# Optimization experiments

Hardware: AMD Instinct MI355X
Metric: run time of the kernel (lower is better)

The kernel has to match this reference:

```python
import jax, jax.numpy as jnp
import numpy as np

D_STATE = 16
D_CONV = 4
DT_RANK = 8


def layer_norm(x, g, b, eps=1e-5):
    m = x.mean(-1, keepdims=True)
    v = ((x - m) ** 2).mean(-1, keepdims=True)
    return (x - m) / jnp.sqrt(v + eps) * g + b


def rms_norm(x, w, eps=1e-5):
    return x * jax.lax.rsqrt(jnp.mean(x * x, -1, keepdims=True) + eps) * w


def mamba_layer(feat, in_proj_w, conv_w, conv_b, x_proj_w, dt_proj_w, dt_proj_b,
                A_log, D_param, out_proj_w, rms_w):
    # feat: [N, C] treated as a length-N sequence with batch 1 (residual block)
    x_in = rms_norm(feat, rms_w)
    xz = x_in @ in_proj_w                         # [N, 2*d_inner]
    d_inner = conv_w.shape[0]
    x, z = xz[:, :d_inner], xz[:, d_inner:]
    # causal depthwise conv1d (torch pad=d_conv-1 then truncate to L)
    L = x.shape[0]
    x_pad = jnp.pad(x, ((D_CONV - 1, 0), (0, 0)))
    xc = conv_b + sum(x_pad[k:k + L, :] * conv_w[:, k] for k in range(D_CONV))
    x = jax.nn.silu(xc)
    dbc = x @ x_proj_w                            # [N, dt_rank + 2*d_state]
    delta = jax.nn.softplus(dbc[:, :DT_RANK] @ dt_proj_w + dt_proj_b)  # [N, d_inner]
    Bm = dbc[:, DT_RANK:DT_RANK + D_STATE]        # [N, d_state]
    Cm = dbc[:, DT_RANK + D_STATE:]               # [N, d_state]
    A = -jnp.exp(A_log)                           # [d_inner, d_state]

    def step(h, inp):
        d_t, b_t, c_t, x_t = inp
        dA = jnp.exp(d_t[:, None] * A)            # [d_inner, d_state]
        h = dA * h + d_t[:, None] * b_t[None, :] * x_t[:, None]
        y_t = (h * c_t[None, :]).sum(-1)          # [d_inner]
        return h, y_t

    h0 = jnp.zeros((d_inner, D_STATE), feat.dtype)
    _, y = jax.lax.scan(step, h0, (delta, Bm, Cm, x))
    y = y + D_param * x
    y = y * jax.nn.silu(z)
    return feat + y @ out_proj_w                  # residual


def setup_inputs() -> dict:
    N, K, C = 32768, 16, 128
    d_inner = 2 * C
    key = jax.random.key(0)
    ks = jax.random.split(key, 12)
    s = 0.02
    inp = {
        "feat": jax.random.normal(ks[0], (N, C), jnp.float32),
        "coord": jax.random.normal(ks[1], (N, 3), jnp.float32),
        "reference_index": jax.random.randint(ks[2], (N, K), 0, N, jnp.int32),
        "gauss_dist": jax.random.uniform(ks[3], (N, K), jnp.float32),
        "j": 0,
        # Mamba params
        "in_proj_w": jax.random.normal(ks[4], (C, 2 * d_inner), jnp.float32) * s,
        "conv_w": jax.random.normal(ks[5], (d_inner, D_CONV), jnp.float32) * s,
        "conv_b": jnp.zeros((d_inner,), jnp.float32),
        "x_proj_w": jax.random.normal(ks[6], (d_inner, DT_RANK + 2 * D_STATE), jnp.float32) * s,
        "dt_proj_w": jax.random.normal(ks[7], (DT_RANK, d_inner), jnp.float32) * s,
        "dt_proj_b": jax.random.uniform(ks[8], (d_inner,), jnp.float32) * 0.1,
        "A_log": jnp.log(jnp.tile(jnp.arange(1.0, D_STATE + 1.0, dtype=jnp.float32), (d_inner, 1))),
        "D_param": jnp.ones((d_inner,), jnp.float32),
        "out_proj_w": jax.random.normal(ks[9], (d_inner, C), jnp.float32) * s,
        "rms_w": jnp.ones((C,), jnp.float32),
        # PointBatchNorm (LayerNorm) shared for both norms
        "ln_g": jnp.ones((C,), jnp.float32),
        "ln_b": jnp.zeros((C,), jnp.float32),
        # linear_attention: Linear(2C->C), LayerNorm, ReLU, Linear(C->C)
        "la_w1": jax.random.normal(ks[10], (2 * C, C), jnp.float32) * s,
        "la_b1": jnp.zeros((C,), jnp.float32),
        "la_ln_g": jnp.ones((C,), jnp.float32),
        "la_ln_b": jnp.zeros((C,), jnp.float32),
        "la_w2": jax.random.normal(ks[11], (C, C), jnp.float32) * s,
        "la_b2": jnp.zeros((C,), jnp.float32),
    }
    return inp


def reference(feat, coord, reference_index, gauss_dist, j,
              in_proj_w, conv_w, conv_b, x_proj_w, dt_proj_w, dt_proj_b,
              A_log, D_param, out_proj_w, rms_w, ln_g, ln_b,
              la_w1, la_b1, la_ln_g, la_ln_b, la_w2, la_b2):
    # pointops.grouping(with_xyz=False): gather neighbor features [N, K, C]
    group_feat = feat[reference_index]
    combined = (gauss_dist[..., None] * group_feat).sum(axis=1)     # [N, C]
    combined = layer_norm(combined, ln_g, ln_b)
    feat_mamba = mamba_layer(feat, in_proj_w, conv_w, conv_b, x_proj_w,
                             dt_proj_w, dt_proj_b, A_log, D_param,
                             out_proj_w, rms_w)
    feat_mamba = layer_norm(feat_mamba, ln_g, ln_b)
    cat_feat = jnp.concatenate([feat_mamba, combined], axis=-1)     # [N, 2C]
    h = jax.nn.relu(layer_norm(cat_feat @ la_w1 + la_b1, la_ln_g, la_ln_b))
    return h @ la_w2 + la_b2
```

## Files before the change

kernel.cpp:

```cpp
#include <hip/hip_runtime.h>
#include <hip/hip_bf16.h>
#include <math.h>

#define N_TOK 32768
#define LC 32
#define NCHUNK (N_TOK / LC)
#define NSEG 64
#define SEGLEN (NCHUNK / NSEG)
#define CXT 16
#define NCXB (N_TOK / CXT)
#define XPAD 264

typedef short short8 __attribute__((ext_vector_type(8)));
typedef float f32x4 __attribute__((ext_vector_type(4)));

__device__ __forceinline__ float siluf_(float v){ return v / (1.f + __expf(-v)); }
__device__ __forceinline__ float softplusf_(float v){ return v > 20.f ? v : __logf(1.f + __expf(v)); }

__device__ __forceinline__ unsigned f2bfu(float f){
  __hip_bfloat16 h = __float2bfloat16(f);
  return (unsigned)*(unsigned short*)&h;
}
__device__ __forceinline__ float bfu2f(unsigned short u){
  __hip_bfloat16 h; *(unsigned short*)&h = u; return __bfloat162float(h);
}

__device__ __forceinline__ float waveRed64(float v){
  #pragma unroll
  for (int m = 1; m < 64; m <<= 1) v += __shfl_xor(v, m);
  return v;
}

__device__ __forceinline__ void pow_chain(float w, float pw[16]){
  pw[0]=w; pw[1]=w*w; pw[2]=pw[1]*w; pw[3]=pw[1]*pw[1];
  pw[4]=pw[3]*pw[0]; pw[5]=pw[3]*pw[1]; pw[6]=pw[3]*pw[2]; pw[7]=pw[3]*pw[3];
  pw[8]=pw[7]*pw[0]; pw[9]=pw[7]*pw[1]; pw[10]=pw[7]*pw[2]; pw[11]=pw[7]*pw[3];
  pw[12]=pw[7]*pw[4]; pw[13]=pw[7]*pw[5]; pw[14]=pw[7]*pw[6]; pw[15]=pw[7]*pw[7];
}

__device__ __forceinline__ bool check_intA(const float aS[16]){
  bool ok = true;
  #pragma unroll
  for (int s=0;s<16;s++){
    float tgt = (float)(s+1);
    if (fabsf(-aS[s] - tgt) > 1e-4f*tgt) ok = false;
  }
  return ok;
}

__global__ void __launch_bounds__(256) k_front(const float* __restrict__ feat,
                        const float* __restrict__ rmsw,
                        unsigned* __restrict__ a0u, unsigned* __restrict__ fb16u,
                        const float* __restrict__ ipw, const float* __restrict__ opw,
                        const float* __restrict__ w1, const float* __restrict__ w2,
                        const float* __restrict__ xpw,
                        __hip_bfloat16* __restrict__ ipwt, __hip_bfloat16* __restrict__ opwt,
                        __hip_bfloat16* __restrict__ w1t, __hip_bfloat16* __restrict__ w2t,
                        __hip_bfloat16* __restrict__ xpwt){
  int bid = blockIdx.x;
  if (bid >= 8192){
    int e = (bid-8192)*256 + threadIdx.x;
    if (e < 65536){ int n=e>>7, k=e&127; ipwt[e]=__float2bfloat16(ipw[k*512+n]); }
    else if (e < 98304){ int f=e-65536; int n=f>>8, k=f&255; opwt[f]=__float2bfloat16(opw[k*128+n]); }
    else if (e < 131072){ int f=e-98304; int n=f>>8, k=f&255; w1t[f]=__float2bfloat16(w1[k*128+n]); }
    else if (e < 147456){ int f=e-131072; int n=f>>7, k=f&127; w2t[f]=__float2bfloat16(w2[k*128+n]); }
    else if (e < 159744){ int f=e-147456; int n=f>>8, k=f&255;
                          xpwt[f]=(n<40)?__float2bfloat16(xpw[k*40+n]):__float2bfloat16(0.f); }
    return;
  }
  int row = bid*4 + (threadIdx.x>>6);
  int lane = threadIdx.x & 63;
  float2 f2 = ((const float2*)feat)[row*64 + lane];
  fb16u[row*64 + lane] = f2bfu(f2.x) | (f2bfu(f2.y) << 16);
  float ss = waveRed64(f2.x*f2.x + f2.y*f2.y);
  float is0 = rsqrtf(ss * (1.f/128.f) + 1e-5f);
  float2 w = ((const float2*)rmsw)[lane];
  a0u[row*64 + lane] = f2bfu(f2.x*is0*w.x) | (f2bfu(f2.y*is0*w.y) << 16);
}

template<int WM16, int WN16>
__global__ __launch_bounds__(256) void k_mfma(const __hip_bfloat16* __restrict__ A,
      const __hip_bfloat16* __restrict__ Wt, int K,
      __hip_bfloat16* __restrict__ out0b, __hip_bfloat16* __restrict__ out1){
  int tid = threadIdx.x;
  int wave = tid>>6, lane = tid&63;
  int wm = wave>>1, wn = wave&1;
  int lane16 = lane&15, quad = lane>>4;
  int m_w = blockIdx.x*(2*WM16*16) + wm*(WM16*16);
  int n_w = blockIdx.y*(2*WN16*16) + wn*(WN16*16);
  f32x4 acc[WM16][WN16];
  #pragma unroll
  for (int i=0;i<WM16;i++)
    #pragma unroll
    for (int j=0;j<WN16;j++) acc[i][j] = (f32x4){0.f,0.f,0.f,0.f};
  const __hip_bfloat16* Ab = A  + (size_t)(m_w + lane16)*K + quad*8;
  const __hip_bfloat16* Bb = Wt + (size_t)(n_w + lane16)*K + quad*8;
  #pragma unroll 4
  for (int kk=0; kk<K; kk+=32){
    short8 a[WM16], b[WN16];
    #pragma unroll
    for (int i=0;i<WM16;i++) a[i] = *(const short8*)(Ab + (size_t)i*16*K + kk);
    #pragma unroll
    for (int j=0;j<WN16;j++) b[j] = *(const short8*)(Bb + (size_t)j*16*K + kk);
    #pragma unroll
    for (int i=0;i<WM16;i++)
      #pragma unroll
      for (int j=0;j<WN16;j++)
        acc[i][j] = __builtin_amdgcn_mfma_f32_16x16x32_bf16(b[j], a[i], acc[i][j], 0, 0, 0);
  }
  #pragma unroll
  for (int i=0;i<WM16;i++){
    int m = m_w + i*16 + lane16;
    #pragma unroll
    for (int j=0;j<WN16;j++){
      int n0 = n_w + j*16 + quad*4;
      if (n0 < 256){
        unsigned u0 = f2bfu(acc[i][j][0]) | (f2bfu(acc[i][j][1]) << 16);
        unsigned u1 = f2bfu(acc[i][j][2]) | (f2bfu(acc[i][j][3]) << 16);
        *(uint2*)(out0b + (size_t)m*256 + n0) = make_uint2(u0, u1);
      } else {
        unsigned u0 = f2bfu(siluf_(acc[i][j][0])) | (f2bfu(siluf_(acc[i][j][1])) << 16);
        unsigned u1 = f2bfu(siluf_(acc[i][j][2])) | (f2bfu(siluf_(acc[i][j][3])) << 16);
        *(uint2*)(out1 + (size_t)m*256 + (n0-256)) = make_uint2(u0, u1);
      }
    }
  }
}

__global__ __launch_bounds__(256) void k_cxd(
      const __hip_bfloat16* __restrict__ bxb,
      const __hip_bfloat16* __restrict__ xpwt,
      const float* __restrict__ cw, const float* __restrict__ cb,
      const float* __restrict__ dtw, const float* __restrict__ dtb,
      unsigned* __restrict__ dxb,
      float* __restrict__ Bm, float* __restrict__ Cm,
      const unsigned* __restrict__ fb16u, const int* __restrict__ ridx,
      const float* __restrict__ gd, const float* __restrict__ g,
      const float* __restrict__ b, unsigned* __restrict__ catB){
  int tid = threadIdx.x;
  int bid = blockIdx.x;

  if (bid >= NCXB){
    int row = (bid - NCXB)*4 + (tid>>6);
    int lane = tid & 63;
    float ax=0.f, ay=0.f;
    #pragma unroll 4
    for (int k=0;k<16;k++){
      int idx = ridx[row*16+k];
      float ww = gd[row*16+k];
      unsigned fu = fb16u[(size_t)idx*64 + lane];
      ax += ww*bfu2f((unsigned short)(fu & 0xffff));
      ay += ww*bfu2f((unsigned short)(fu >> 16));
    }
    float m = waveRed64(ax+ay) * (1.f/128.f);
    float dx = ax-m, dy = ay-m;
    float var = waveRed64(dx*dx+dy*dy) * (1.f/128.f);
    float is = rsqrtf(var + 1e-5f);
    float2 gg = ((const float2*)g)[lane];
    float2 bb = ((const float2*)b)[lane];
    float ox = dx*is*gg.x + bb.x, oy = dy*is*gg.y + bb.y;
    catB[row*64 + lane] = f2bfu(ox) | (f2bfu(oy) << 16);
    return;
  }

  __shared__ __align__(16) __hip_bfloat16 Xs[CXT][XPAD];
  __shared__ __align__(16) float DT[CXT][8];
  int wave = tid>>6, lane = tid&63;
  int lane16 = lane&15, quad = lane>>4;
  int r0 = bid*CXT;

  {
    int d = tid;
    float cw0=cw[d*4], cw1=cw[d*4+1], cw2=cw[d*4+2], cw3=cw[d*4+3], cbb=cb[d];
    float a_0 = (r0 >= 3) ? __bfloat162float(bxb[(size_t)(r0-3)*256 + d]) : 0.f;
    float a_1 = (r0 >= 2) ? __bfloat162float(bxb[(size_t)(r0-2)*256 + d]) : 0.f;
    float a_2 = (r0 >= 1) ? __bfloat162float(bxb[(size_t)(r0-1)*256 + d]) : 0.f;
    #pragma unroll 4
    for (int t=0;t<CXT;t++){
      float a_3 = __bfloat162float(bxb[(size_t)(r0+t)*256 + d]);
      float xc = siluf_(cbb + cw0*a_0 + cw1*a_1 + cw2*a_2 + cw3*a_3);
      Xs[t][d] = __float2bfloat16(xc);
      a_0=a_1; a_1=a_2; a_2=a_3;
    }
  }
  __syncthreads();

  if (wave < 3){
    f32x4 acc3 = (f32x4){0.f,0.f,0.f,0.f};
    const __hip_bfloat16* Arow = &Xs[lane16][0] + quad*8;
    const __hip_bfloat16* Bb = xpwt + (size_t)(wave*16 + lane16)*256 + quad*8;
    #pragma unroll
    for (int kk=0; kk<256; kk+=32){
      short8 a  = *(const short8*)(Arow + kk);
      short8 bfr = *(const short8*)(Bb + kk);
      acc3 = __builtin_amdgcn_mfma_f32_16x16x32_bf16(a, bfr, acc3, 0, 0, 0);
    }
    int n = wave*16 + lane16;
    #pragma unroll
    for (int r=0;r<4;r++){
      int m = quad*4 + r;
      float v = acc3[r];
      if (n < 8)       DT[m][n] = v;
      else if (n < 24) Bm[(size_t)(r0+m)*16 + (n-8)] = v;
      else if (n < 40) Cm[(size_t)(r0+m)*16 + (n-24)] = v;
    }
  }
  __syncthreads();

  {
    int d = tid;
    float w8[8];
    #pragma unroll
    for (int j=0;j<8;j++) w8[j] = dtw[j*256+d];
    float dbias = dtb[d];
    #pragma unroll
    for (int t=0;t<CXT;t++){
      const float4* T = (const float4*)&DT[t][0];
      float4 u = T[0], v = T[1];
      float acc = dbias
        + u.x*w8[0] + u.y*w8[1] + u.z*w8[2] + u.w*w8[3]
        + v.x*w8[4] + v.y*w8[5] + v.z*w8[6] + v.w*w8[7];
      float dv = softplusf_(acc);
      unsigned xu = *(const unsigned short*)&Xs[t][d];
      dxb[(size_t)(r0+t)*256 + d] = f2bfu(dv) | (xu << 16);
    }
  }
}

__global__ __launch_bounds__(256) void k_scan1(const unsigned* __restrict__ dxb,
      const float* __restrict__ Bm, const float* __restrict__ A_log,
      float* __restrict__ dsum_o, __hip_bfloat16* __restrict__ Hc){
  __shared__ float Bl[LC][16];
  int g = blockIdx.x;
  int tid = threadIdx.x;
  int d = tid;
  int t0 = g*LC;
  if (tid < LC*4) ((float4*)&Bl[0][0])[tid] = ((const float4*)(Bm + (size_t)t0*16))[tid];
  __syncthreads();
  float aS[16];
  #pragma unroll
  for (int s=0;s<16;s++) aS[s] = -__expf(A_log[d*16+s]);
  bool fastA = check_intA(aS);
  float h[16] = {};
  float dsum = 0.f;
  if (fastA){
    #pragma unroll 4
    for (int t=0;t<LC;t++){
      unsigned u = dxb[(size_t)(t0+t)*256 + d];
      float dv = bfu2f((unsigned short)(u & 0xffff));
      float xv = bfu2f((unsigned short)(u >> 16));
      const float4* Bp = (const float4*)&Bl[t][0];
      float4 b0=Bp[0], b1=Bp[1], b2=Bp[2], b3=Bp[3];
      float bl[16] = {b0.x,b0.y,b0.z,b0.w, b1.x,b1.y,b1.z,b1.w,
                      b2.x,b2.y,b2.z,b2.w, b3.x,b3.y,b3.z,b3.w};
      dsum += dv;
      float dx_ = dv*xv;
      float w[16]; pow_chain(__expf(-dv), w);
      #pragma unroll
      for (int s=0;s<16;s++) h[s] = w[s]*h[s] + dx_*bl[s];
    }
  } else {
    #pragma unroll 4
    for (int t=0;t<LC;t++){
      unsigned u = dxb[(size_t)(t0+t)*256 + d];
      float dv = bfu2f((unsigned short)(u & 0xffff));
      float xv = bfu2f((unsigned short)(u >> 16));
      const float4* Bp = (const float4*)&Bl[t][0];
      float4 b0=Bp[0], b1=Bp[1], b2=Bp[2], b3=Bp[3];
      float bl[16] = {b0.x,b0.y,b0.z,b0.w, b1.x,b1.y,b1.z,b1.w,
                      b2.x,b2.y,b2.z,b2.w, b3.x,b3.y,b3.z,b3.w};
      dsum += dv;
      float dx_ = dv*xv;
      #pragma unroll
      for (int s=0;s<16;s++) h[s] = __expf(dv*aS[s])*h[s] + dx_*bl[s];
    }
  }
  dsum_o[(size_t)g*256 + d] = dsum;
  unsigned u[8];
  #pragma unroll
  for (int q=0;q<8;q++) u[q] = f2bfu(h[2*q]) | (f2bfu(h[2*q+1]) << 16);
  uint4* Hd = (uint4*)(Hc + (size_t)g*4096 + (size_t)d*16);
  Hd[0] = make_uint4(u[0],u[1],u[2],u[3]);
  Hd[1] = make_uint4(u[4],u[5],u[6],u[7]);
}

__global__ __launch_bounds__(256) void k_carry_a(const float* __restrict__ dsum,
      __hip_bfloat16* __restrict__ Hc, const float* __restrict__ A_log,
      float* __restrict__ dsum_pre, float* __restrict__ segsum, float* __restrict__ Hagg){
  int seg = blockIdx.x;
  int ch  = blockIdx.y*256 + threadIdx.x;
  int d = ch>>4, s = ch&15;
  float aSv = -__expf(A_log[ch]);
  float dpre = 0.f, c = 0.f;
  int g0 = seg*SEGLEN;
  #pragma unroll 4
  for (int i=0;i<SEGLEN;i++){
    int g = g0+i;
    float ds = dsum[(size_t)g*256 + d];
    size_t a = (size_t)g*4096 + ch;
    float hh = __bfloat162float(Hc[a]);
    float p = __expf(ds*aSv);
    if (s==0) dsum_pre[(size_t)g*256 + d] = dpre;
    Hc[a] = __float2bfloat16(c);
    dpre += ds;
    c = p*c + hh;
  }
  if (s==0) segsum[seg*256 + d] = dpre;
  Hagg[(size_t)seg*4096 + ch] = c;
}

__global__ __launch_bounds__(256) void k_carry_b(const float* __restrict__ segsum,
      const float* __restrict__ Hagg, const float* __restrict__ A_log,
      float* __restrict__ Cseg){
  int ch = blockIdx.x*256 + threadIdx.x;
  int d = ch>>4;
  float aSv = -__expf(A_log[ch]);
  float c = 0.f;
  #pragma unroll 8
  for (int s=0;s<NSEG;s++){
    Cseg[(size_t)s*4096 + ch] = c;
    c = __expf(segsum[s*256 + d]*aSv)*c + Hagg[(size_t)s*4096 + ch];
  }
}

__global__ __launch_bounds__(256) void k_scan2(const unsigned* __restrict__ dxb,
      const __hip_bfloat16* __restrict__ zb, const float* __restrict__ Bm,
      const float* __restrict__ Cm, const float* __restrict__ A_log,
      const float* __restrict__ Dp, const float* __restrict__ dsum_pre,
      const __hip_bfloat16* __restrict__ Hc, const float* __restrict__ Cseg,
      __hip_bfloat16* __restrict__ yb){
  __shared__ float Bl[LC][16];
  __shared__ float Cl[LC][16];
  int g = blockIdx.x;
  int tid = threadIdx.x;
  int d = tid;
  int t0 = g*LC;
  if (tid < 128) ((float4*)&Bl[0][0])[tid] = ((const float4*)(Bm + (size_t)t0*16))[tid];
  else ((float4*)&Cl[0][0])[tid-128] = ((const float4*)(Cm + (size_t)t0*16))[tid-128];
  __syncthreads();
  int seg = g / SEGLEN;
  float aS[16];
  #pragma unroll
  for (int s=0;s<16;s++) aS[s] = -__expf(A_log[d*16+s]);
  bool fastA = check_intA(aS);
  float h[16];
  {
    float dpre = dsum_pre[(size_t)g*256 + d];
    const uint4* hp = (const uint4*)(Hc + (size_t)g*4096 + (size_t)d*16);
    uint4 H0 = hp[0], H1 = hp[1];
    unsigned hu[8] = {H0.x,H0.y,H0.z,H0.w, H1.x,H1.y,H1.z,H1.w};
    const float4* cs = (const float4*)(Cseg + (size_t)seg*4096 + (size_t)d*16);
    float ws[16];
    if (fastA){
      pow_chain(__expf(-dpre), ws);
    } else {
      #pragma unroll
      for (int s=0;s<16;s++) ws[s] = __expf(dpre*aS[s]);
    }
    #pragma unroll
    for (int q=0;q<4;q++){
      float4 C = cs[q];
      h[q*4+0] = ws[q*4+0]*C.x + bfu2f((unsigned short)(hu[q*2]   & 0xffff));
      h[q*4+1] = ws[q*4+1]*C.y + bfu2f((unsigned short)(hu[q*2]   >> 16));
      h[q*4+2] = ws[q*4+2]*C.z + bfu2f((unsigned short)(hu[q*2+1] & 0xffff));
      h[q*4+3] = ws[q*4+3]*C.w + bfu2f((unsigned short)(hu[q*2+1] >> 16));
    }
  }
  float dpar = Dp[d];
  if (fastA){
    #pragma unroll 4
    for (int t=0;t<LC;t++){
      unsigned u = dxb[(size_t)(t0+t)*256 + d];
      float dv = bfu2f((unsigned short)(u & 0xffff));
      float xv = bfu2f((unsigned short)(u >> 16));
      float zv = __bfloat162float(zb[(size_t)(t0+t)*256 + d]);
      const float4* Bp = (const float4*)&Bl[t][0];
      const float4* Cp = (const float4*)&Cl[t][0];
      float4 b0=Bp[0], b1=Bp[1], b2=Bp[2], b3=Bp[3];
      float4 c0=Cp[0], c1=Cp[1], c2=Cp[2], c3=Cp[3];
      float bl[16] = {b0.x,b0.y,b0.z,b0.w, b1.x,b1.y,b1.z,b1.w,
                      b2.x,b2.y,b2.z,b2.w, b3.x,b3.y,b3.z,b3.w};
      float cl[16] = {c0.x,c0.y,c0.z,c0.w, c1.x,c1.y,c1.z,c1.w,
                      c2.x,c2.y,c2.z,c2.w, c3.x,c3.y,c3.z,c3.w};
      float dx_ = dv*xv;
      float w[16]; pow_chain(__expf(-dv), w);
      float yv = 0.f;
      #pragma unroll
      for (int s=0;s<16;s++){
        h[s] = w[s]*h[s] + dx_*bl[s];
        yv += h[s]*cl[s];
      }
      yb[(size_t)(t0+t)*256 + d] = __float2bfloat16((yv + dpar*xv)*zv);
    }
  } else {
    #pragma unroll 4
    for (int t=0;t<LC;t++){
      unsigned u = dxb[(size_t)(t0+t)*256 + d];
      float dv = bfu2f((unsigned short)(u & 0xffff));
      float xv = bfu2f((unsigned short)(u >> 16));
      float zv = __bfloat162float(zb[(size_t)(t0+t)*256 + d]);
      const float4* Bp = (const float4*)&Bl[t][0];
      const float4* Cp = (const float4*)&Cl[t][0];
      float4 b0=Bp[0], b1=Bp[1], b2=Bp[2], b3=Bp[3];
      float4 c0=Cp[0], c1=Cp[1], c2=Cp[2], c3=Cp[3];
      float bl[16] = {b0.x,b0.y,b0.z,b0.w, b1.x,b1.y,b1.z,b1.w,
                      b2.x,b2.y,b2.z,b2.w, b3.x,b3.y,b3.z,b3.w};
      float cl[16] = {c0.x,c0.y,c0.z,c0.w, c1.x,c1.y,c1.z,c1.w,
                      c2.x,c2.y,c2.z,c2.w, c3.x,c3.y,c3.z,c3.w};
      float dx_ = dv*xv;
      float yv = 0.f;
      #pragma unroll
      for (int s=0;s<16;s++){
        h[s] = __expf(dv*aS[s])*h[s] + dx_*bl[s];
        yv += h[s]*cl[s];
      }
      yb[(size_t)(t0+t)*256 + d] = __float2bfloat16((yv + dpar*xv)*zv);
    }
  }
}

__global__ __launch_bounds__(256) void k_tail(const __hip_bfloat16* __restrict__ yb,
      const __hip_bfloat16* __restrict__ opwt, const float* __restrict__ feat,
      const float* __restrict__ lng, const float* __restrict__ lnb,
      const unsigned* __restrict__ catB,
      const __hip_bfloat16* __restrict__ w1t, const float* __restrict__ b1,
      const float* __restrict__ lag, const float* __restrict__ lab,
      const __hip_bfloat16* __restrict__ w2t, const float* __restrict__ b2,
      float* __restrict__ out){
  __shared__ __align__(16) float Ls[64][132];
  __shared__ __align__(16) unsigned Cu[64][132];
  int tid = threadIdx.x;
  int wave = tid>>6, lane = tid&63;
  int wm = wave>>1, wn = wave&1;
  int lane16 = lane&15, quad = lane>>4;
  int r0 = blockIdx.x*64;

  #pragma unroll
  for (int i=0;i<16;i++){
    int idx = i*256 + tid;
    int row = idx>>6, c = idx&63;
    Cu[row][64+c] = catB[(size_t)(r0+row)*64 + c];
  }

  f32x4 acc[2][4];
  #pragma unroll
  for (int i=0;i<2;i++)
    #pragma unroll
    for (int j=0;j<4;j++) acc[i][j] = (f32x4){0.f,0.f,0.f,0.f};
  {
    const __hip_bfloat16* Ab = yb   + (size_t)(r0 + wm*32 + lane16)*256 + quad*8;
    const __hip_bfloat16* Bb = opwt + (size_t)(wn*64 + lane16)*256 + quad*8;
    #pragma unroll 2
    for (int kk=0; kk<256; kk+=32){
      short8 a[2], bf[4];
      #pragma unroll
      for (int i=0;i<2;i++) a[i] = *(const short8*)(Ab + (size_t)i*16*256 + kk);
      #pragma unroll
      for (int j=0;j<4;j++) bf[j] = *(const short8*)(Bb + (size_t)j*16*256 + kk);
      #pragma unroll
      for (int i=0;i<2;i++)
        #pragma unroll
        for (int j=0;j<4;j++)
          acc[i][j] = __builtin_amdgcn_mfma_f32_16x16x32_bf16(a[i], bf[j], acc[i][j], 0, 0, 0);
    }
  }
  #pragma unroll
  for (int i=0;i<2;i++)
    #pragma unroll
    for (int j=0;j<4;j++){
      int n = wn*64 + j*16 + lane16;
      #pragma unroll
      for (int r=0;r<4;r++){
        int m = wm*32 + i*16 + quad*4 + r;
        Ls[m][n] = acc[i][j][r] + feat[(size_t)(r0+m)*128 + n];
      }
    }
  __syncthreads();
  {
    float2 gv = ((const float2*)lng)[lane];
    float2 bv = ((const float2*)lnb)[lane];
    #pragma unroll 4
    for (int rr=0; rr<16; rr++){
      int row = wave*16 + rr;
      float2 v = *(const float2*)&Ls[row][2*lane];
      float mm = waveRed64(v.x+v.y) * (1.f/128.f);
      float dx = v.x-mm, dy = v.y-mm;
      float var = waveRed64(dx*dx+dy*dy) * (1.f/128.f);
      float is = rsqrtf(var + 1e-5f);
      Cu[row][lane] = f2bfu(dx*is*gv.x + bv.x) | (f2bfu(dy*is*gv.y + bv.y) << 16);
    }
  }
  __syncthreads();
  #pragma unroll
  for (int i=0;i<2;i++)
    #pragma unroll
    for (int j=0;j<4;j++) acc[i][j] = (f32x4){0.f,0.f,0.f,0.f};
  {
    const __hip_bfloat16* Bb = w1t + (size_t)(wn*64 + lane16)*256 + quad*8;
    #pragma unroll 2
    for (int kk=0; kk<256; kk+=32){
      short8 a[2], bf[4];
      #pragma unroll
      for (int i=0;i<2;i++)
        a[i] = *(const short8*)(&Cu[wm*32 + i*16 + lane16][0] + (kk>>1) + quad*4);
      #pragma unroll
      for (int j=0;j<4;j++) bf[j] = *(const short8*)(Bb + (size_t)j*16*256 + kk);
      #pragma unroll
      for (int i=0;i<2;i++)
        #pragma unroll
        for (int j=0;j<4;j++)
          acc[i][j] = __builtin_amdgcn_mfma_f32_16x16x32_bf16(a[i], bf[j], acc[i][j], 0, 0, 0);
    }
  }
  #pragma unroll
  for (int i=0;i<2;i++)
    #pragma unroll
    for (int j=0;j<4;j++){
      int n = wn*64 + j*16 + lane16;
      float bv1 = b1[n];
      #pragma unroll
      for (int r=0;r<4;r++){
        int m = wm*32 + i*16 + quad*4 + r;
        Ls[m][n] = acc[i][j][r] + bv1;
      }
    }
  __syncthreads();
  {
    float2 gv = ((const float2*)lag)[lane];
    float2 bv = ((const float2*)lab)[lane];
    #pragma unroll 4
    for (int rr=0; rr<16; rr++){
      int row = wave*16 + rr;
      float2 v = *(const float2*)&Ls[row][2*lane];
      float mm = waveRed64(v.x+v.y) * (1.f/128.f);
      float dx = v.x-mm, dy = v.y-mm;
      float var = waveRed64(dx*dx+dy*dy) * (1.f/128.f);
      float is = rsqrtf(var + 1e-5f);
      float ox = fmaxf(dx*is*gv.x + bv.x, 0.f);
      float oy = fmaxf(dy*is*gv.y + bv.y, 0.f);
      Cu[row][lane] = f2bfu(ox) | (f2bfu(oy) << 16);
    }
  }
  __syncthreads();
  #pragma unroll
  for (int i=0;i<2;i++)
    #pragma unroll
    for (int j=0;j<4;j++) acc[i][j] = (f32x4){0.f,0.f,0.f,0.f};
  {
    const __hip_bfloat16* Bb = w2t + (size_t)(wn*64 + lane16)*128 + quad*8;
    #pragma unroll
    for (int kk=0; kk<128; kk+=32){
      short8 a[2], bf[4];
      #pragma unroll
      for (int i=0;i<2;i++)
        a[i] = *(const short8*)(&Cu[wm*32 + i*16 + lane16][0] + (kk>>1) + quad*4);
      #pragma unroll
      for (int j=0;j<4;j++) bf[j] = *(const short8*)(Bb + (size_t)j*16*128 + kk);
      #pragma unroll
      for (int i=0;i<2;i++)
        #pragma unroll
        for (int j=0;j<4;j++)
          acc[i][j] = __builtin_amdgcn_mfma_f32_16x16x32_bf16(bf[j], a[i], acc[i][j], 0, 0, 0);
    }
  }
  #pragma unroll
  for (int i=0;i<2;i++){
    int m = wm*32 + i*16 + lane16;
    #pragma unroll
    for (int j=0;j<4;j++){
      int n0 = wn*64 + j*16 + quad*4;
      float4 o;
      o.x = acc[i][j][0] + b2[n0+0];
      o.y = acc[i][j][1] + b2[n0+1];
      o.z = acc[i][j][2] + b2[n0+2];
      o.w = acc[i][j][3] + b2[n0+3];
      *(float4*)(out + (size_t)(r0+m)*128 + n0) = o;
    }
  }
}

extern "C" void kernel_launch(void* const* d_in, const int* in_sizes, int n_in,
                              void* d_out, int out_size, void* d_ws, size_t ws_size,
                              hipStream_t stream){
  const float* feat = (const float*)d_in[0];
  const int*   ridx = (const int*)d_in[2];
  const float* gd   = (const float*)d_in[3];
  const float* ipw  = (const float*)d_in[5];
  const float* cw   = (const float*)d_in[6];
  const float* cb   = (const float*)d_in[7];
  const float* xpw  = (const float*)d_in[8];
  const float* dtw  = (const float*)d_in[9];
  const float* dtb  = (const float*)d_in[10];
  const float* alog = (const float*)d_in[11];
  const float* dpar = (const float*)d_in[12];
  const float* opw  = (const float*)d_in[13];
  const float* rmsw = (const float*)d_in[14];
  const float* lng  = (const float*)d_in[15];
  const float* lnb  = (const float*)d_in[16];
  const float* w1   = (const float*)d_in[17];
  const float* b1   = (const float*)d_in[18];
  const float* lag  = (const float*)d_in[19];
  const float* lab  = (const float*)d_in[20];
  const float* w2   = (const float*)d_in[21];
  const float* b2   = (const float*)d_in[22];
  float* out = (float*)d_out;

  char* p = (char*)d_ws;
  __hip_bfloat16* bxb  = (__hip_bfloat16*)p; p += (size_t)N_TOK*256*2;
  __hip_bfloat16* zb   = (__hip_bfloat16*)p; p += (size_t)N_TOK*256*2;
  unsigned* dxb        = (unsigned*)p;       p += (size_t)N_TOK*256*4;
  unsigned* catB       = (unsigned*)p;       p += (size_t)N_TOK*64*4;
  unsigned* fb16u      = (unsigned*)p;       p += (size_t)N_TOK*64*4;
  __hip_bfloat16* yb   = (__hip_bfloat16*)p; p += (size_t)N_TOK*256*2;
  float* Bm   = (float*)p; p += (size_t)N_TOK*16*4;
  float* Cm   = (float*)p; p += (size_t)N_TOK*16*4;
  __hip_bfloat16* Hc = (__hip_bfloat16*)p; p += (size_t)NCHUNK*4096*2;
  float* dsum = (float*)p; p += (size_t)NCHUNK*256*4;
  float* dpre = (float*)p; p += (size_t)NCHUNK*256*4;
  float* segs = (float*)p; p += (size_t)NSEG*256*4;
  float* Hagg = (float*)p; p += (size_t)NSEG*4096*4;
  float* Cseg = (float*)p; p += (size_t)NSEG*4096*4;
  __hip_bfloat16* ipwt = (__hip_bfloat16*)p; p += 512*128*2;
  __hip_bfloat16* opwt = (__hip_bfloat16*)p; p += 128*256*2;
  __hip_bfloat16* w1t  = (__hip_bfloat16*)p; p += 128*256*2;
  __hip_bfloat16* w2t  = (__hip_bfloat16*)p; p += 128*128*2;
  __hip_bfloat16* xpwt = (__hip_bfloat16*)p; p += 48*256*2;
  __hip_bfloat16* a0 = yb;

  hipLaunchKernelGGL(k_front, dim3(8192+624), dim3(256), 0, stream,
                     feat, rmsw, (unsigned*)a0, fb16u,
                     ipw, opw, w1, w2, xpw, ipwt, opwt, w1t, w2t, xpwt);
  hipLaunchKernelGGL((k_mfma<4,4>), dim3(N_TOK/128, 4), dim3(256), 0, stream,
                     a0, ipwt, 128, bxb, zb);
  hipLaunchKernelGGL(k_cxd, dim3(NCXB + 8192), dim3(256), 0, stream,
                     bxb, xpwt, cw, cb, dtw, dtb, dxb, Bm, Cm,
                     fb16u, ridx, gd, lng, lnb, catB);
  hipLaunchKernelGGL(k_scan1, dim3(NCHUNK), dim3(256), 0, stream,
                     dxb, Bm, alog, dsum, Hc);
  hipLaunchKernelGGL(k_carry_a, dim3(NSEG, 16), dim3(256), 0, stream,
                     dsum, Hc, alog, dpre, segs, Hagg);
  hipLaunchKernelGGL(k_carry_b, dim3(16), dim3(256), 0, stream, segs, Hagg, alog, Cseg);
  hipLaunchKernelGGL(k_scan2, dim3(NCHUNK), dim3(256), 0, stream,
                     dxb, zb, Bm, Cm, alog, dpar, dpre, Hc, Cseg, yb);
  hipLaunchKernelGGL(k_tail, dim3(N_TOK/64), dim3(256), 0, stream,
                     yb, opwt, feat, lng, lnb, catB, w1t, b1, lag, lab, w2t, b2, out);
}
```

Before: 266.2 us.

## Split neighbor gather-layernorm work across cxd, scan1 and scan2 kernels

The neighbor gather plus layernorm was appended entirely as extra blocks of the conv/dt kernel. It is now split into 2048, 4096 and 2048 groups of four rows, attached to k_cxd, k_scan1 and k_scan2. The scan kernels launch only 1024 chunk blocks, which underfill the GPU, so the independent gather blocks can fill idle compute units and overlap with the latency-bound scans. The risk is that gather blocks compete with scan blocks for bandwidth and scheduling slots, which could lengthen the critical scan path.

```diff
diff --git a/kernel.cpp b/kernel.cpp
--- a/kernel.cpp
+++ b/kernel.cpp
@@ -9,6 +9,10 @@
 #define SEGLEN (NCHUNK / NSEG)
 #define CXT 16
 #define NCXB (N_TOK / CXT)
+#define NGRP 8192
+#define G_CXD 2048
+#define G_S1  4096
+#define G_S2  2048
 #define XPAD 264
 
 typedef short short8 __attribute__((ext_vector_type(8)));
@@ -46,6 +50,31 @@
     if (fabsf(-aS[s] - tgt) > 1e-4f*tgt) ok = false;
   }
   return ok;
+}
+
+__device__ __forceinline__ void gather_ln(int grp, int tid,
+      const unsigned* __restrict__ fb16u, const int* __restrict__ ridx,
+      const float* __restrict__ gd, const float* __restrict__ g,
+      const float* __restrict__ b, unsigned* __restrict__ catB){
+  int row = grp*4 + (tid>>6);
+  int lane = tid & 63;
+  float ax=0.f, ay=0.f;
+  #pragma unroll 4
+  for (int k=0;k<16;k++){
+    int idx = ridx[row*16+k];
+    float ww = gd[row*16+k];
+    unsigned fu = fb16u[(size_t)idx*64 + lane];
+    ax += ww*bfu2f((unsigned short)(fu & 0xffff));
+    ay += ww*bfu2f((unsigned short)(fu >> 16));
+  }
+  float m = waveRed64(ax+ay) * (1.f/128.f);
+  float dx = ax-m, dy = ay-m;
+  float var = waveRed64(dx*dx+dy*dy) * (1.f/128.f);
+  float is = rsqrtf(var + 1e-5f);
+  float2 gg = ((const float2*)g)[lane];
+  float2 bb = ((const float2*)b)[lane];
+  float ox = dx*is*gg.x + bb.x, oy = dy*is*gg.y + bb.y;
+  catB[row*64 + lane] = f2bfu(ox) | (f2bfu(oy) << 16);
 }
 
 __global__ void __launch_bounds__(256) k_front(const float* __restrict__ feat,
@@ -141,25 +170,7 @@
   int bid = blockIdx.x;
 
   if (bid >= NCXB){
-    int row = (bid - NCXB)*4 + (tid>>6);
-    int lane = tid & 63;
-    float ax=0.f, ay=0.f;
-    #pragma unroll 4
-    for (int k=0;k<16;k++){
-      int idx = ridx[row*16+k];
-      float ww = gd[row*16+k];
-      unsigned fu = fb16u[(size_t)idx*64 + lane];
-      ax += ww*bfu2f((unsigned short)(fu & 0xffff));
-      ay += ww*bfu2f((unsigned short)(fu >> 16));
-    }
-    float m = waveRed64(ax+ay) * (1.f/128.f);
-    float dx = ax-m, dy = ay-m;
-    float var = waveRed64(dx*dx+dy*dy) * (1.f/128.f);
-    float is = rsqrtf(var + 1e-5f);
-    float2 gg = ((const float2*)g)[lane];
-    float2 bb = ((const float2*)b)[lane];
-    float ox = dx*is*gg.x + bb.x, oy = dy*is*gg.y + bb.y;
-    catB[row*64 + lane] = f2bfu(ox) | (f2bfu(oy) << 16);
+    gather_ln(bid - NCXB, tid, fb16u, ridx, gd, g, b, catB);
     return;
   }
 
@@ -229,12 +240,19 @@
 
 __global__ __launch_bounds__(256) void k_scan1(const unsigned* __restrict__ dxb,
       const float* __restrict__ Bm, const float* __restrict__ A_log,
-      float* __restrict__ dsum_o, __hip_bfloat16* __restrict__ Hc){
+      float* __restrict__ dsum_o, __hip_bfloat16* __restrict__ Hc,
+      const unsigned* __restrict__ fb16u, const int* __restrict__ ridx,
+      const float* __restrict__ gd, const float* __restrict__ g,
+      const float* __restrict__ b, unsigned* __restrict__ catB){
   __shared__ float Bl[LC][16];
-  int g = blockIdx.x;
+  int g_ = blockIdx.x;
   int tid = threadIdx.x;
+  if (g_ >= NCHUNK){
+    gather_ln(G_CXD + (g_ - NCHUNK), tid, fb16u, ridx, gd, g, b, catB);
+    return;
+  }
   int d = tid;
-  int t0 = g*LC;
+  int t0 = g_*LC;
   if (tid < LC*4) ((float4*)&Bl[0][0])[tid] = ((const float4*)(Bm + (size_t)t0*16))[tid];
   __syncthreads();
   float aS[16];
@@ -275,11 +293,11 @@
       for (int s=0;s<16;s++) h[s] = __expf(dv*aS[s])*h[s] + dx_*bl[s];
     }
   }
-  dsum_o[(size_t)g*256 + d] = dsum;
+  dsum_o[(size_t)g_*256 + d] = dsum;
   unsigned u[8];
   #pragma unroll
   for (int q=0;q<8;q++) u[q] = f2bfu(h[2*q]) | (f2bfu(h[2*q+1]) << 16);
-  uint4* Hd = (uint4*)(Hc + (size_t)g*4096 + (size_t)d*16);
+  uint4* Hd = (uint4*)(Hc + (size_t)g_*4096 + (size_t)d*16);
   Hd[0] = make_uint4(u[0],u[1],u[2],u[3]);
   Hd[1] = make_uint4(u[4],u[5],u[6],u[7]);
 }
@@ -328,25 +346,32 @@
       const float* __restrict__ Cm, const float* __restrict__ A_log,
       const float* __restrict__ Dp, const float* __restrict__ dsum_pre,
       const __hip_bfloat16* __restrict__ Hc, const float* __restrict__ Cseg,
-      __hip_bfloat16* __restrict__ yb){
+      __hip_bfloat16* __restrict__ yb,
+      const unsigned* __restrict__ fb16u, const int* __restrict__ ridx,
+      const float* __restrict__ gd, const float* __restrict__ g,
+      const float* __restrict__ b, unsigned* __restrict__ catB){
   __shared__ float Bl[LC][16];
   __shared__ float Cl[LC][16];
-  int g = blockIdx.x;
+  int g_ = blockIdx.x;
   int tid = threadIdx.x;
+  if (g_ >= NCHUNK){
+    gather_ln(G_CXD + G_S1 + (g_ - NCHUNK), tid, fb16u, ridx, gd, g, b, catB);
+    return;
+  }
   int d = tid;
-  int t0 = g*LC;
+  int t0 = g_*LC;
   if (tid < 128) ((float4*)&Bl[0][0])[tid] = ((const float4*)(Bm + (size_t)t0*16))[tid];
   else ((float4*)&Cl[0][0])[tid-128] = ((const float4*)(Cm + (size_t)t0*16))[tid-128];
   __syncthreads();
-  int seg = g / SEGLEN;
+  int seg = g_ / SEGLEN;
   float aS[16];
   #pragma unroll
   for (int s=0;s<16;s++) aS[s] = -__expf(A_log[d*16+s]);
   bool fastA = check_intA(aS);
   float h[16];
   {
-    float dpre = dsum_pre[(size_t)g*256 + d];
-    const uint4* hp = (const uint4*)(Hc + (size_t)g*4096 + (size_t)d*16);
+    float dpre = dsum_pre[(size_t)g_*256 + d];
+    const uint4* hp = (const uint4*)(Hc + (size_t)g_*4096 + (size_t)d*16);
     uint4 H0 = hp[0], H1 = hp[1];
     unsigned hu[8] = {H0.x,H0.y,H0.z,H0.w, H1.x,H1.y,H1.z,H1.w};
     const float4* cs = (const float4*)(Cseg + (size_t)seg*4096 + (size_t)d*16);
@@ -632,16 +657,18 @@
                      ipw, opw, w1, w2, xpw, ipwt, opwt, w1t, w2t, xpwt);
   hipLaunchKernelGGL((k_mfma<4,4>), dim3(N_TOK/128, 4), dim3(256), 0, stream,
                      a0, ipwt, 128, bxb, zb);
-  hipLaunchKernelGGL(k_cxd, dim3(NCXB + 8192), dim3(256), 0, stream,
+  hipLaunchKernelGGL(k_cxd, dim3(NCXB + G_CXD), dim3(256), 0, stream,
                      bxb, xpwt, cw, cb, dtw, dtb, dxb, Bm, Cm,
                      fb16u, ridx, gd, lng, lnb, catB);
-  hipLaunchKernelGGL(k_scan1, dim3(NCHUNK), dim3(256), 0, stream,
-                     dxb, Bm, alog, dsum, Hc);
+  hipLaunchKernelGGL(k_scan1, dim3(NCHUNK + G_S1), dim3(256), 0, stream,
+                     dxb, Bm, alog, dsum, Hc,
+                     fb16u, ridx, gd, lng, lnb, catB);
   hipLaunchKernelGGL(k_carry_a, dim3(NSEG, 16), dim3(256), 0, stream,
                      dsum, Hc, alog, dpre, segs, Hagg);
   hipLaunchKernelGGL(k_carry_b, dim3(16), dim3(256), 0, stream, segs, Hagg, alog, Cseg);
-  hipLaunchKernelGGL(k_scan2, dim3(NCHUNK), dim3(256), 0, stream,
-                     dxb, zb, Bm, Cm, alog, dpar, dpre, Hc, Cseg, yb);
+  hipLaunchKernelGGL(k_scan2, dim3(NCHUNK + G_S2), dim3(256), 0, stream,
+                     dxb, zb, Bm, Cm, alog, dpar, dpre, Hc, Cseg, yb,
+                     fb16u, ridx, gd, lng, lnb, catB);
   hipLaunchKernelGGL(k_tail, dim3(N_TOK/64), dim3(256), 0, stream,
                      yb, opwt, feat, lng, lnb, catB, w1t, b1, lag, lab, w2t, b2, out);
 }
```

Result: no change. 265.8 us (-0.1%).
